# Kernel optimization log

Hardware: AMD Instinct MI355X
Metric: run time of the kernel (lower is better)

## Reference

```python
import jax, jax.numpy as jnp
import numpy as np

BETA = 0.95
THRESH = 1.0
T = 25
MAXD = 11      # dilated_kernel_size: 250//25=10 -> bumped to odd 11
LP = 10        # left_pad = 250//25
B = 1024
SIGINIT = 5.0  # max_delay // 2, SIG is frozen at this value


@jax.custom_vjp
def atan_spike(u):
    # heaviside forward, atan surrogate gradient (snntorch surrogate.atan, alpha=2)
    return (u > 0).astype(u.dtype)

def _atan_fwd(u):
    return atan_spike(u), u

def _atan_bwd(u, g):
    return (g / (1.0 + (jnp.pi * u) ** 2),)

atan_spike.defvjp(_atan_fwd, _atan_bwd)


def dcls_kernel(W, P, SIG):
    # DCLS 'gauss': gaussian-interpolated dense kernel.
    # W: (O, I, kc), P/SIG: (1, O, I, kc) -> dense kernel (O, I, MAXD)
    idx = jnp.arange(MAXD, dtype=W.dtype)
    Pc = P[0] + MAXD // 2                      # center positions in dense kernel
    S = jnp.abs(SIG[0]) + 0.27                 # sigma floor (DCLS epsilon)
    X = jnp.exp(-0.5 * ((idx[:, None, None, None] - Pc) / S) ** 2)  # (K,O,I,kc)
    X = X / (X.sum(axis=0, keepdims=True) + 1e-7)
    return jnp.einsum('oic,joic->oij', W, X)


def dcls_conv(x, W, P, SIG, b):
    # x: (B, C_in, L) -> (B, C_out, L - MAXD + 1), VALID conv like padding=0
    k = dcls_kernel(W, P, SIG)
    y = jax.lax.conv_general_dilated(x, k, (1,), 'VALID',
                                     dimension_numbers=('NCH', 'OIH', 'NCH'))
    return y + b[None, :, None]


def batchnorm(x, gamma, beta, mean, var, eps=1e-5):
    # eval-mode BatchNorm1d over (B, C, L)
    inv = gamma / jnp.sqrt(var + eps)
    return (x - mean[None, :, None]) * inv[None, :, None] + beta[None, :, None]


def lif_scan(x):
    # snntorch Leaky, reset_mechanism='subtract'; x: (B, C, T) input currents
    xT = jnp.moveaxis(x, 2, 0)  # (T, B, C)

    def step(mem, xt):
        reset = jax.lax.stop_gradient(atan_spike(mem - THRESH))  # detached reset
        mem = BETA * mem + xt - reset * THRESH
        spk = atan_spike(mem - THRESH)
        return mem, (spk, mem)

    _, (spk, mem) = jax.lax.scan(step, jnp.zeros_like(xT[0]), xT)
    return spk, mem  # each (T, B, C)


def pad_left(x):
    return jnp.pad(x, ((0, 0), (0, 0), (LP, 0)))


def setup_inputs() -> dict:
    key = jax.random.key(0)
    ks = jax.random.split(key, 16)

    def w_init(k, o, i):
        return jax.random.normal(k, (o, i, 1), jnp.float32) / np.sqrt(i)

    inp = {
        'data': jax.random.normal(ks[0], (B, T, 140), jnp.float32),
        'W1': w_init(ks[1], 256, 140),
        'b1': jax.random.normal(ks[2], (256,), jnp.float32) * 0.01,
        'P1': jax.random.uniform(ks[3], (1, 256, 140, 1), jnp.float32, -SIGINIT, SIGINIT),
        'SIG1': jnp.full((1, 256, 140, 1), SIGINIT, jnp.float32),
        'bn1_gamma': jax.random.uniform(ks[4], (256,), jnp.float32, 0.5, 1.5),
        'bn1_beta': jax.random.normal(ks[5], (256,), jnp.float32) * 0.1,
        'bn1_mean': jax.random.normal(ks[6], (256,), jnp.float32) * 0.1,
        'bn1_var': jax.random.uniform(ks[7], (256,), jnp.float32, 0.5, 1.5),
        'W2': w_init(ks[8], 256, 256),
        'b2': jax.random.normal(ks[9], (256,), jnp.float32) * 0.01,
        'P2': jax.random.uniform(ks[10], (1, 256, 256, 1), jnp.float32, -SIGINIT, SIGINIT),
        'SIG2': jnp.full((1, 256, 256, 1), SIGINIT, jnp.float32),
        'bn2_gamma': jax.random.uniform(ks[11], (256,), jnp.float32, 0.5, 1.5),
        'bn2_beta': jax.random.normal(ks[12], (256,), jnp.float32) * 0.1,
        'bn2_mean': jax.random.normal(ks[13], (256,), jnp.float32) * 0.1,
        'bn2_var': jax.random.uniform(ks[14], (256,), jnp.float32, 0.5, 1.5),
        'W3': w_init(ks[15], 20, 256),
        'b3': jnp.zeros((20,), jnp.float32),
        'P3': jax.random.uniform(jax.random.fold_in(key, 99), (1, 20, 256, 1), jnp.float32, -SIGINIT, SIGINIT),
        'SIG3': jnp.full((1, 20, 256, 1), SIGINIT, jnp.float32),
    }
    return inp


def reference(data, W1, b1, P1, SIG1, bn1_gamma, bn1_beta, bn1_mean, bn1_var,
              W2, b2, P2, SIG2, bn2_gamma, bn2_beta, bn2_mean, bn2_var,
              W3, b3, P3, SIG3):
    # data: (B, T, 140); pad time dim on the left, then to (B, C, L)
    x = jnp.moveaxis(jnp.pad(data, ((0, 0), (LP, 0), (0, 0))), 1, 2)  # (B,140,T+LP)
    x = batchnorm(dcls_conv(x, W1, P1, SIG1, b1), bn1_gamma, bn1_beta, bn1_mean, bn1_var)
    spk1, _ = lif_scan(x)                  # (T, B, 256)
    in1 = jnp.moveaxis(spk1, 0, 2)         # (B, 256, T)  (dropout eval = identity)

    x = batchnorm(dcls_conv(pad_left(in1), W2, P2, SIG2, b2),
                  bn2_gamma, bn2_beta, bn2_mean, bn2_var)
    spk2, _ = lif_scan(x)
    in2 = jnp.moveaxis(spk2, 0, 2)         # (B, 256, T)

    x = dcls_conv(pad_left(in2), W3, P3, SIG3, b3)  # (B, 20, T)
    spk3, mem3 = lif_scan(x)               # (T, B, 20) each
    return spk3, mem3
```

## Files before the change

kernel.cpp:

```cpp
#include <hip/hip_runtime.h>
#include <math.h>

#define BB 1024
#define TT 25
#define LP 10
#define MAXD 11

#define XR2 26
#define XC 264
#define XSZ2 (XR2 * XC)

#define IC1 140
#define ICP1 160
#define XC1 168
#define XSZ1 (XR2 * XC1)
#define SS1 (2 * XSZ1)

typedef __bf16 bf16x8 __attribute__((ext_vector_type(8)));
typedef float  f32x4  __attribute__((ext_vector_type(4)));

#define MFMA16(A, B, C) __builtin_amdgcn_mfma_f32_16x16x32_bf16((A), (B), (C), 0, 0, 0)

__global__ void gen_trip(const float* __restrict__ W,
                         const float* __restrict__ P,
                         const float* __restrict__ SIG,
                         __bf16* __restrict__ Khi, __bf16* __restrict__ Kmid,
                         __bf16* __restrict__ Klo,
                         int O, int Opad, int I, int Ipad) {
    int idx = blockIdx.x * blockDim.x + threadIdx.x;
    if (idx >= Opad * Ipad) return;
    int i = idx % Ipad;
    int o = idx / Ipad;
    if (o >= O || i >= I) {
#pragma unroll
        for (int j = 0; j < MAXD; ++j) {
            size_t ofs = ((size_t)(j * Opad + o)) * Ipad + i;
            Khi[ofs] = (__bf16)0.0f;
            Kmid[ofs] = (__bf16)0.0f;
            Klo[ofs] = (__bf16)0.0f;
        }
        return;
    }
    int widx = o * I + i;
    float w  = W[widx];
    float pc = P[widx] + (float)(MAXD / 2);
    float s  = fabsf(SIG[widx]) + 0.27f;
    float x[MAXD];
    float sum = 0.f;
#pragma unroll
    for (int j = 0; j < MAXD; ++j) {
        float d = ((float)j - pc) / s;
        x[j] = expf(-0.5f * d * d);
        sum += x[j];
    }
    float denom = sum + 1e-7f;
#pragma unroll
    for (int j = 0; j < MAXD; ++j) {
        float kv = w * (x[j] / denom);
        __bf16 h = (__bf16)kv;
        float  r1 = kv - (float)h;
        __bf16 m = (__bf16)r1;
        float  r2 = r1 - (float)m;
        __bf16 l = (__bf16)r2;
        size_t ofs = ((size_t)(j * Opad + o)) * Ipad + i;
        Khi[ofs] = h;
        Kmid[ofs] = m;
        Klo[ofs] = l;
    }
}

__global__ __launch_bounds__(512, 2)
void conv1_mfma(const float* __restrict__ xin,
                const __bf16* __restrict__ Khi,
                const __bf16* __restrict__ Kmid,
                const __bf16* __restrict__ Klo,
                const float* __restrict__ bias,
                const float* __restrict__ gamma,
                const float* __restrict__ beta,
                const float* __restrict__ mean,
                const float* __restrict__ var,
                __bf16* __restrict__ spk1) {
    __shared__ __align__(16) char smem[3 * SS1 * 2];
    __bf16* xs = (__bf16*)smem;
    float*  ys = (float*)smem;

    const int rr = blockIdx.x & 7;
    const int gg = blockIdx.x >> 3;
    const int pp = 2 * (rr + 8 * (gg >> 1)) + (gg & 1);
    const int b0 = pp * 2;

    const int tid  = threadIdx.x;
    const int w    = tid >> 6;
    const int lane = tid & 63;
    const int lm   = lane & 15;
    const int quad = lane >> 4;

    {
        uint32_t* xz = (uint32_t*)smem;
        for (int k = tid; k < 3 * SS1 / 2; k += 512) xz[k] = 0u;
    }
    __syncthreads();
#pragma unroll
    for (int bl = 0; bl < 2; ++bl) {
        const float* src = xin + (size_t)(b0 + bl) * (TT * IC1);
        for (int k = tid; k < TT * IC1; k += 512) {
            int t = k / IC1;
            int i = k - t * IC1;
            float x  = src[k];
            __bf16 h = (__bf16)x;
            float r1 = x - (float)h;
            __bf16 m = (__bf16)r1;
            float r2 = r1 - (float)m;
            __bf16 l = (__bf16)r2;
            int ofs = bl * XSZ1 + t * XC1 + i;
            xs[0 * SS1 + ofs] = h;
            xs[1 * SS1 + ofs] = m;
            xs[2 * SS1 + ofs] = l;
        }
    }
    __syncthreads();

    f32x4 acc[2][4];
#pragma unroll
    for (int p = 0; p < 2; ++p)
#pragma unroll
        for (int nt = 0; nt < 4; ++nt) acc[p][nt] = (f32x4){0.f, 0.f, 0.f, 0.f};

    auto loadA = [&](int n, bf16x8* Ah, bf16x8* Am, bf16x8* Al) {
        n = (n > 54) ? 54 : n;
        const int j = n / 5;
        const int ic = n - 5 * j;
        const size_t base =
            (size_t)(j * 256 + w * 32 + lm) * ICP1 + ic * 32 + quad * 8;
#pragma unroll
        for (int p = 0; p < 2; ++p) {
            Ah[p] = *(const bf16x8*)(Khi  + base + p * 16 * ICP1);
            Am[p] = *(const bf16x8*)(Kmid + base + p * 16 * ICP1);
            Al[p] = *(const bf16x8*)(Klo  + base + p * 16 * ICP1);
        }
    };

    auto step = [&](int n, bf16x8* Ah, bf16x8* Am, bf16x8* Al) {
        const int j = n / 5;
        const int ic = n - 5 * j;
        int r0 = lm + j - 10;          r0 = ((unsigned)r0 < 25u) ? r0 : 25;
        int r1 = 16 + lm + j - 10;     r1 = ((unsigned)r1 < 25u) ? r1 : 25;
        const int col = ic * 32 + quad * 8;
#pragma unroll
        for (int bl = 0; bl < 2; ++bl) {
            bf16x8 Bh[2], Bm[2], Bl[2];
#pragma unroll
            for (int th = 0; th < 2; ++th) {
                const int row = th ? r1 : r0;
                const int ofs = bl * XSZ1 + row * XC1 + col;
                Bh[th] = *(const bf16x8*)&xs[0 * SS1 + ofs];
                Bm[th] = *(const bf16x8*)&xs[1 * SS1 + ofs];
                Bl[th] = *(const bf16x8*)&xs[2 * SS1 + ofs];
            }
#pragma unroll
            for (int p = 0; p < 2; ++p)
#pragma unroll
                for (int th = 0; th < 2; ++th)
                    acc[p][bl * 2 + th] = MFMA16(Ah[p], Bh[th], acc[p][bl * 2 + th]);
#pragma unroll
            for (int p = 0; p < 2; ++p)
#pragma unroll
                for (int th = 0; th < 2; ++th)
                    acc[p][bl * 2 + th] = MFMA16(Ah[p], Bm[th], acc[p][bl * 2 + th]);
#pragma unroll
            for (int p = 0; p < 2; ++p)
#pragma unroll
                for (int th = 0; th < 2; ++th)
                    acc[p][bl * 2 + th] = MFMA16(Am[p], Bh[th], acc[p][bl * 2 + th]);
#pragma unroll
            for (int p = 0; p < 2; ++p)
#pragma unroll
                for (int th = 0; th < 2; ++th)
                    acc[p][bl * 2 + th] = MFMA16(Ah[p], Bl[th], acc[p][bl * 2 + th]);
#pragma unroll
            for (int p = 0; p < 2; ++p)
#pragma unroll
                for (int th = 0; th < 2; ++th)
                    acc[p][bl * 2 + th] = MFMA16(Am[p], Bm[th], acc[p][bl * 2 + th]);
#pragma unroll
            for (int p = 0; p < 2; ++p)
#pragma unroll
                for (int th = 0; th < 2; ++th)
                    acc[p][bl * 2 + th] = MFMA16(Al[p], Bh[th], acc[p][bl * 2 + th]);
        }
    };

    bf16x8 A0h[2], A0m[2], A0l[2], A1h[2], A1m[2], A1l[2];
    loadA(0, A0h, A0m, A0l);
    for (int n = 0; n < 54; n += 2) {
        loadA(n + 1, A1h, A1m, A1l);
        step(n, A0h, A0m, A0l);
        loadA(n + 2, A0h, A0m, A0l);
        step(n + 1, A1h, A1m, A1l);
    }
    step(54, A0h, A0m, A0l);

#pragma unroll
    for (int bl = 0; bl < 2; ++bl) {
        __syncthreads();
#pragma unroll
        for (int p = 0; p < 2; ++p)
#pragma unroll
            for (int th = 0; th < 2; ++th) {
                int t = th * 16 + lm;
                if (t < TT) {
                    int ob = w * 32 + p * 16 + quad * 4;
#pragma unroll
                    for (int v = 0; v < 4; ++v)
                        ys[(ob + v) * 27 + t] = acc[p][bl * 2 + th][v];
                }
            }
        __syncthreads();
        if (tid < 256) {
            const int o = tid;
            float scale = gamma[o] / sqrtf(var[o] + 1e-5f);
            float ofs   = (bias[o] - mean[o]) * scale + beta[o];
            unsigned short* dst =
                (unsigned short*)spk1 + (size_t)(b0 + bl) * (TT * 256) + o;
            const float* yrow = &ys[o * 27];
            float memv = 0.f;
#pragma unroll
            for (int t = 0; t < TT; ++t) {
                float a     = yrow[t] * scale + ofs;
                float reset = (memv > 1.0f) ? 1.0f : 0.f;
                memv        = 0.95f * memv + a - reset;
                dst[t * 256] = (memv > 1.0f) ? 0x3F80 : 0;
            }
        }
    }
}

__global__ __launch_bounds__(512, 2)
void conv2_mfma(const __bf16* __restrict__ spk1,
                const __bf16* __restrict__ Khi,
                const __bf16* __restrict__ Kmid,
                const __bf16* __restrict__ Klo,
                const float* __restrict__ bias,
                const float* __restrict__ gamma,
                const float* __restrict__ beta,
                const float* __restrict__ mean,
                const float* __restrict__ var,
                __bf16* __restrict__ spk2) {
    __shared__ __align__(16) char smem[116480];
    __bf16* xs  = (__bf16*)smem;
    float*  ysq = (float*)(smem + 109824);

    const int h    = blockIdx.x & 1;
    const int bg   = blockIdx.x >> 1;
    const int b0   = bg * 8;
    const int oc0  = h * 128;

    const int tid  = threadIdx.x;
    const int w    = tid >> 6;
    const int wc   = w & 3;
    const int wb   = w >> 2;
    const int lane = tid & 63;
    const int lm   = lane & 15;
    const int quad = lane >> 4;

    for (int k = tid; k < 8 * (XC / 2); k += 512) {
        int bl = k / (XC / 2);
        int c  = k % (XC / 2);
        ((uint32_t*)xs)[(bl * XSZ2 + 25 * XC) / 2 + c] = 0u;
    }
    for (int k = tid; k < 8 * 800; k += 512) {
        int bl = k / 800;
        int v  = k % 800;
        int t  = v >> 5;
        int iv = v & 31;
        uint4 d = ((const uint4*)(spk1 + (size_t)(b0 + bl) * (TT * 256)))[v];
        *(uint4*)&xs[bl * XSZ2 + t * XC + iv * 8] = d;
    }
    __syncthreads();

    f32x4 acc[2][8];
#pragma unroll
    for (int pi = 0; pi < 2; ++pi)
#pragma unroll
        for (int nt = 0; nt < 8; ++nt) acc[pi][nt] = (f32x4){0.f, 0.f, 0.f, 0.f};

    {
        auto loadA = [&](int n, bf16x8* Ah, bf16x8* Am, bf16x8* Al) {
            n = (n > 87) ? 87 : n;
            const int j = n >> 3, ic = n & 7;
#pragma unroll
            for (int pi = 0; pi < 2; ++pi) {
                const size_t base =
                    (size_t)(j * 256 + oc0 + wc * 32 + pi * 16 + lm) * 256 +
                    ic * 32 + quad * 8;
                Ah[pi] = *(const bf16x8*)(Khi  + base);
                Am[pi] = *(const bf16x8*)(Kmid + base);
                Al[pi] = *(const bf16x8*)(Klo  + base);
            }
        };
        auto step = [&](int n, bf16x8* Ah, bf16x8* Am, bf16x8* Al) {
            const int j = n >> 3, ic = n & 7;
            int r0 = lm + j - 10;          r0 = ((unsigned)r0 < 25u) ? r0 : 25;
            int r1 = 16 + lm + j - 10;     r1 = ((unsigned)r1 < 25u) ? r1 : 25;
            const int col = ic * 32 + quad * 8;
            bf16x8 Bf[8];
#pragma unroll
            for (int bl = 0; bl < 4; ++bl) {
                const int xb = wb * 4 + bl;
                Bf[bl * 2 + 0] = *(const bf16x8*)&xs[xb * XSZ2 + r0 * XC + col];
                Bf[bl * 2 + 1] = *(const bf16x8*)&xs[xb * XSZ2 + r1 * XC + col];
            }
#pragma unroll
            for (int pi = 0; pi < 2; ++pi)
#pragma unroll
                for (int nt = 0; nt < 8; ++nt)
                    acc[pi][nt] = MFMA16(Ah[pi], Bf[nt], acc[pi][nt]);
#pragma unroll
            for (int pi = 0; pi < 2; ++pi)
#pragma unroll
                for (int nt = 0; nt < 8; ++nt)
                    acc[pi][nt] = MFMA16(Am[pi], Bf[nt], acc[pi][nt]);
#pragma unroll
            for (int pi = 0; pi < 2; ++pi)
#pragma unroll
                for (int nt = 0; nt < 8; ++nt)
                    acc[pi][nt] = MFMA16(Al[pi], Bf[nt], acc[pi][nt]);
        };

        bf16x8 A0h[2], A0m[2], A0l[2], A1h[2], A1m[2], A1l[2];
        loadA(0, A0h, A0m, A0l);
        for (int n = 0; n < 86; n += 2) {
            loadA(n + 1, A1h, A1m, A1l);
            step(n, A0h, A0m, A0l);
            loadA(n + 2, A0h, A0m, A0l);
            step(n + 1, A1h, A1m, A1l);
        }
        loadA(87, A1h, A1m, A1l);
        step(86, A0h, A0m, A0l);
        step(87, A1h, A1m, A1l);
    }

#pragma unroll
    for (int blg = 0; blg < 8; ++blg) {
#pragma unroll
        for (int q = 0; q < 2; ++q) {
            __syncthreads();
            if (wb == (blg >> 2) && (wc >> 1) == q) {
#pragma unroll
                for (int pi = 0; pi < 2; ++pi)
#pragma unroll
                    for (int th = 0; th < 2; ++th) {
                        int t = th * 16 + lm;
                        if (t < TT) {
                            int ol = (wc & 1) * 32 + pi * 16 + quad * 4;
#pragma unroll
                            for (int v = 0; v < 4; ++v)
                                ysq[(ol + v) * 26 + t] =
                                    acc[pi][(blg & 3) * 2 + th][v];
                        }
                    }
            }
            __syncthreads();
            if (tid < 64) {
                const int o = oc0 + q * 64 + tid;
                float scale = gamma[o] / sqrtf(var[o] + 1e-5f);
                float ofs   = (bias[o] - mean[o]) * scale + beta[o];
                const float* yrow = &ysq[tid * 26];
                unsigned short* dst =
                    (unsigned short*)spk2 + (size_t)(b0 + blg) * (TT * 256) + o;
                float memv = 0.f;
#pragma unroll
                for (int t = 0; t < TT; ++t) {
                    float a     = yrow[t] * scale + ofs;
                    float reset = (memv > 1.0f) ? 1.0f : 0.f;
                    memv        = 0.95f * memv + a - reset;
                    dst[t * 256] = (memv > 1.0f) ? 0x3F80 : 0;
                }
            }
        }
    }
}

__global__ __launch_bounds__(512, 2)
void conv3_mfma(const __bf16* __restrict__ spk2,
                const __bf16* __restrict__ K3hi,
                const __bf16* __restrict__ K3mid,
                const __bf16* __restrict__ K3lo,
                const float* __restrict__ b3,
                float* __restrict__ out) {
    __shared__ __align__(16) char smem[54912];
    __bf16* xs  = (__bf16*)smem;
    float*  ys3 = (float*)smem;

    const int b0   = blockIdx.x * 4;
    const int tid  = threadIdx.x;
    const int w    = tid >> 6;
    const int lane = tid & 63;
    const int lm   = lane & 15;
    const int quad = lane >> 4;

    for (int k = tid; k < 4 * (XC / 2); k += 512) {
        int bl = k / (XC / 2);
        int c  = k % (XC / 2);
        ((uint32_t*)xs)[(bl * XSZ2 + 25 * XC) / 2 + c] = 0u;
    }
    for (int k = tid; k < 4 * 800; k += 512) {
        int bl = k / 800;
        int v  = k % 800;
        int t  = v >> 5;
        int iv = v & 31;
        uint4 d = ((const uint4*)(spk2 + (size_t)(b0 + bl) * (TT * 256)))[v];
        *(uint4*)&xs[bl * XSZ2 + t * XC + iv * 8] = d;
    }
    __syncthreads();

    {
        const int p3  = w >> 2;
        const int bl3 = w & 3;
        f32x4 accH[2], accM[2], accL[2];
#pragma unroll
        for (int th = 0; th < 2; ++th) {
            accH[th] = (f32x4){0.f, 0.f, 0.f, 0.f};
            accM[th] = (f32x4){0.f, 0.f, 0.f, 0.f};
            accL[th] = (f32x4){0.f, 0.f, 0.f, 0.f};
        }

        auto loadA3 = [&](int n, bf16x8* Ah, bf16x8* Am, bf16x8* Al) {
            n = (n > 87) ? 87 : n;
            const int j = n >> 3, ic = n & 7;
            const size_t kofs =
                ((size_t)(j * 32 + p3 * 16 + lm)) * 256 + ic * 32 + quad * 8;
            *Ah = *(const bf16x8*)(K3hi  + kofs);
            *Am = *(const bf16x8*)(K3mid + kofs);
            *Al = *(const bf16x8*)(K3lo  + kofs);
        };
        auto step3 = [&](int n, bf16x8 Ah, bf16x8 Am, bf16x8 Al) {
            const int j = n >> 3, ic = n & 7;
#pragma unroll
            for (int th = 0; th < 2; ++th) {
                int r = th * 16 + lm + j - 10;
                r = ((unsigned)r < 25u) ? r : 25;
                bf16x8 Bf =
                    *(const bf16x8*)&xs[bl3 * XSZ2 + r * XC + ic * 32 + quad * 8];
                accH[th] = MFMA16(Ah, Bf, accH[th]);
                accM[th] = MFMA16(Am, Bf, accM[th]);
                accL[th] = MFMA16(Al, Bf, accL[th]);
            }
        };

        bf16x8 A0h, A0m, A0l, A1h, A1m, A1l;
        loadA3(0, &A0h, &A0m, &A0l);
        for (int n = 0; n < 86; n += 2) {
            loadA3(n + 1, &A1h, &A1m, &A1l);
            step3(n, A0h, A0m, A0l);
            loadA3(n + 2, &A0h, &A0m, &A0l);
            step3(n + 1, A1h, A1m, A1l);
        }
        loadA3(87, &A1h, &A1m, &A1l);
        step3(86, A0h, A0m, A0l);
        step3(87, A1h, A1m, A1l);

        __syncthreads();
#pragma unroll
        for (int th = 0; th < 2; ++th) {
            int t = th * 16 + lm;
            if (t < TT) {
#pragma unroll
                for (int v = 0; v < 4; ++v)
                    ys3[(bl3 * 32 + p3 * 16 + quad * 4 + v) * 26 + t] =
                        accH[th][v] + accM[th][v] + accL[th][v];
            }
        }
        __syncthreads();

        if (tid < 80) {
            const int bl2 = tid / 20;
            const int o   = tid % 20;
            float memv = 0.f;
            float bo   = b3[o];
            const float* yrow = &ys3[(bl2 * 32 + o) * 26];
#pragma unroll
            for (int t = 0; t < TT; ++t) {
                float a     = yrow[t] + bo;
                float reset = (memv > 1.0f) ? 1.0f : 0.f;
                memv        = 0.95f * memv + a - reset;
                float spk   = (memv > 1.0f) ? 1.0f : 0.f;
                out[(t * BB + (b0 + bl2)) * 20 + o]               = spk;
                out[TT * BB * 20 + (t * BB + (b0 + bl2)) * 20 + o] = memv;
            }
        }
    }
}

extern "C" void kernel_launch(void* const* d_in, const int* in_sizes, int n_in,
                              void* d_out, int out_size, void* d_ws, size_t ws_size,
                              hipStream_t stream) {
    const float* data = (const float*)d_in[0];
    const float* W1   = (const float*)d_in[1];
    const float* b1   = (const float*)d_in[2];
    const float* P1   = (const float*)d_in[3];
    const float* SIG1 = (const float*)d_in[4];
    const float* g1   = (const float*)d_in[5];
    const float* be1  = (const float*)d_in[6];
    const float* m1   = (const float*)d_in[7];
    const float* v1   = (const float*)d_in[8];
    const float* W2   = (const float*)d_in[9];
    const float* b2   = (const float*)d_in[10];
    const float* P2   = (const float*)d_in[11];
    const float* SIG2 = (const float*)d_in[12];
    const float* g2   = (const float*)d_in[13];
    const float* be2  = (const float*)d_in[14];
    const float* m2   = (const float*)d_in[15];
    const float* v2   = (const float*)d_in[16];
    const float* W3   = (const float*)d_in[17];
    const float* b3   = (const float*)d_in[18];
    const float* P3   = (const float*)d_in[19];
    const float* SIG3 = (const float*)d_in[20];
    float* out = (float*)d_out;

    char* p = (char*)d_ws;
    __bf16* K1hi  = (__bf16*)p;  p += 901120;
    __bf16* K1mid = (__bf16*)p;  p += 901120;
    __bf16* K1lo  = (__bf16*)p;  p += 901120;
    __bf16* spk1  = (__bf16*)p;  p += 13107200;
    __bf16* K2hi  = (__bf16*)p;  p += 1441792;
    __bf16* K2mid = (__bf16*)p;  p += 1441792;
    __bf16* K2lo  = (__bf16*)p;  p += 1441792;
    __bf16* K3hi  = (__bf16*)p;  p += 180224;
    __bf16* K3mid = (__bf16*)p;  p += 180224;
    __bf16* K3lo  = (__bf16*)p;  p += 180224;
    __bf16* spk2  = (__bf16*)p;

    gen_trip<<<(256 * 160 + 255) / 256, 256, 0, stream>>>(
        W1, P1, SIG1, K1hi, K1mid, K1lo, 256, 256, 140, 160);
    gen_trip<<<(256 * 256 + 255) / 256, 256, 0, stream>>>(
        W2, P2, SIG2, K2hi, K2mid, K2lo, 256, 256, 256, 256);
    gen_trip<<<(32 * 256 + 255) / 256, 256, 0, stream>>>(
        W3, P3, SIG3, K3hi, K3mid, K3lo, 20, 32, 256, 256);

    conv1_mfma<<<BB / 2, 512, 0, stream>>>(data, K1hi, K1mid, K1lo,
                                           b1, g1, be1, m1, v1, spk1);
    conv2_mfma<<<BB / 4, 512, 0, stream>>>(spk1, K2hi, K2mid, K2lo,
                                           b2, g2, be2, m2, v2, spk2);
    conv3_mfma<<<BB / 4, 512, 0, stream>>>(spk2, K3hi, K3mid, K3lo, b3, out);
}
```

Measured before the change: 432.1 us.

## Split conv2 reduction across wave groups with 4-batch blocks and more occupancy

conv2 now handles 4 batch rows per block instead of 8, launches twice as many blocks, and splits the 88-step K reduction between two wave groups. Their partial sums are added in shared memory before the LIF scan. Shared memory drops from about 116KB to 68KB and launch bounds rise to 4 blocks per CU, aiming for more concurrent waves and better latency hiding. The explicit double-buffered A-fragment prefetch is removed in favour of loads interleaved between MFMA groups. Each weight fragment is now reused across fewer batches, so more global weight traffic is needed per unit of work.

Measured after the change: 465.5 us. 1.08x slower.

```diff
diff --git a/kernel.cpp b/kernel.cpp
--- a/kernel.cpp
+++ b/kernel.cpp
@@ -235,7 +235,7 @@
     }
 }
 
-__global__ __launch_bounds__(512, 2)
+__global__ __launch_bounds__(512, 4)
 void conv2_mfma(const __bf16* __restrict__ spk1,
                 const __bf16* __restrict__ Khi,
                 const __bf16* __restrict__ Kmid,
@@ -246,29 +246,29 @@
                 const float* __restrict__ mean,
                 const float* __restrict__ var,
                 __bf16* __restrict__ spk2) {
-    __shared__ __align__(16) char smem[116480];
+    __shared__ __align__(16) char smem[68224];
     __bf16* xs  = (__bf16*)smem;
-    float*  ysq = (float*)(smem + 109824);
+    float*  ysq = (float*)(smem + 54912);
 
     const int h    = blockIdx.x & 1;
     const int bg   = blockIdx.x >> 1;
-    const int b0   = bg * 8;
+    const int b0   = bg * 4;
     const int oc0  = h * 128;
 
     const int tid  = threadIdx.x;
     const int w    = tid >> 6;
     const int wc   = w & 3;
-    const int wb   = w >> 2;
+    const int kg   = w >> 2;
     const int lane = tid & 63;
     const int lm   = lane & 15;
     const int quad = lane >> 4;
 
-    for (int k = tid; k < 8 * (XC / 2); k += 512) {
+    for (int k = tid; k < 4 * (XC / 2); k += 512) {
         int bl = k / (XC / 2);
         int c  = k % (XC / 2);
         ((uint32_t*)xs)[(bl * XSZ2 + 25 * XC) / 2 + c] = 0u;
     }
-    for (int k = tid; k < 8 * 800; k += 512) {
+    for (int k = tid; k < 4 * 800; k += 512) {
         int bl = k / 800;
         int v  = k % 800;
         int t  = v >> 5;
@@ -285,20 +285,9 @@
         for (int nt = 0; nt < 8; ++nt) acc[pi][nt] = (f32x4){0.f, 0.f, 0.f, 0.f};
 
     {
-        auto loadA = [&](int n, bf16x8* Ah, bf16x8* Am, bf16x8* Al) {
-            n = (n > 87) ? 87 : n;
-            const int j = n >> 3, ic = n & 7;
-#pragma unroll
-            for (int pi = 0; pi < 2; ++pi) {
-                const size_t base =
-                    (size_t)(j * 256 + oc0 + wc * 32 + pi * 16 + lm) * 256 +
-                    ic * 32 + quad * 8;
-                Ah[pi] = *(const bf16x8*)(Khi  + base);
-                Am[pi] = *(const bf16x8*)(Kmid + base);
-                Al[pi] = *(const bf16x8*)(Klo  + base);
-            }
-        };
-        auto step = [&](int n, bf16x8* Ah, bf16x8* Am, bf16x8* Al) {
+        const int n0 = kg * 44;
+#pragma unroll 2
+        for (int n = n0; n < n0 + 44; ++n) {
             const int j = n >> 3, ic = n & 7;
             int r0 = lm + j - 10;          r0 = ((unsigned)r0 < 25u) ? r0 : 25;
             int r1 = 16 + lm + j - 10;     r1 = ((unsigned)r1 < 25u) ? r1 : 25;
@@ -306,10 +295,15 @@
             bf16x8 Bf[8];
 #pragma unroll
             for (int bl = 0; bl < 4; ++bl) {
-                const int xb = wb * 4 + bl;
-                Bf[bl * 2 + 0] = *(const bf16x8*)&xs[xb * XSZ2 + r0 * XC + col];
-                Bf[bl * 2 + 1] = *(const bf16x8*)&xs[xb * XSZ2 + r1 * XC + col];
-            }
+                Bf[bl * 2 + 0] = *(const bf16x8*)&xs[bl * XSZ2 + r0 * XC + col];
+                Bf[bl * 2 + 1] = *(const bf16x8*)&xs[bl * XSZ2 + r1 * XC + col];
+            }
+            const size_t base =
+                (size_t)(j * 256 + oc0 + wc * 32 + lm) * 256 + ic * 32 + quad * 8;
+            bf16x8 Ah[2], Am[2], Al[2];
+#pragma unroll
+            for (int pi = 0; pi < 2; ++pi)
+                Ah[pi] = *(const bf16x8*)(Khi + base + pi * 16 * 256);
 #pragma unroll
             for (int pi = 0; pi < 2; ++pi)
 #pragma unroll
@@ -317,35 +311,29 @@
                     acc[pi][nt] = MFMA16(Ah[pi], Bf[nt], acc[pi][nt]);
 #pragma unroll
             for (int pi = 0; pi < 2; ++pi)
+                Am[pi] = *(const bf16x8*)(Kmid + base + pi * 16 * 256);
+#pragma unroll
+            for (int pi = 0; pi < 2; ++pi)
 #pragma unroll
                 for (int nt = 0; nt < 8; ++nt)
                     acc[pi][nt] = MFMA16(Am[pi], Bf[nt], acc[pi][nt]);
 #pragma unroll
             for (int pi = 0; pi < 2; ++pi)
+                Al[pi] = *(const bf16x8*)(Klo + base + pi * 16 * 256);
+#pragma unroll
+            for (int pi = 0; pi < 2; ++pi)
 #pragma unroll
                 for (int nt = 0; nt < 8; ++nt)
                     acc[pi][nt] = MFMA16(Al[pi], Bf[nt], acc[pi][nt]);
-        };
-
-        bf16x8 A0h[2], A0m[2], A0l[2], A1h[2], A1m[2], A1l[2];
-        loadA(0, A0h, A0m, A0l);
-        for (int n = 0; n < 86; n += 2) {
-            loadA(n + 1, A1h, A1m, A1l);
-            step(n, A0h, A0m, A0l);
-            loadA(n + 2, A0h, A0m, A0l);
-            step(n + 1, A1h, A1m, A1l);
-        }
-        loadA(87, A1h, A1m, A1l);
-        step(86, A0h, A0m, A0l);
-        step(87, A1h, A1m, A1l);
-    }
-
-#pragma unroll
-    for (int blg = 0; blg < 8; ++blg) {
+        }
+    }
+
+#pragma unroll
+    for (int bl = 0; bl < 4; ++bl) {
 #pragma unroll
         for (int q = 0; q < 2; ++q) {
             __syncthreads();
-            if (wb == (blg >> 2) && (wc >> 1) == q) {
+            if ((wc >> 1) == q) {
 #pragma unroll
                 for (int pi = 0; pi < 2; ++pi)
 #pragma unroll
@@ -355,8 +343,8 @@
                             int ol = (wc & 1) * 32 + pi * 16 + quad * 4;
 #pragma unroll
                             for (int v = 0; v < 4; ++v)
-                                ysq[(ol + v) * 26 + t] =
-                                    acc[pi][(blg & 3) * 2 + th][v];
+                                ysq[(kg * 64 + ol + v) * 26 + t] =
+                                    acc[pi][bl * 2 + th][v];
                         }
                     }
             }
@@ -365,13 +353,14 @@
                 const int o = oc0 + q * 64 + tid;
                 float scale = gamma[o] / sqrtf(var[o] + 1e-5f);
                 float ofs   = (bias[o] - mean[o]) * scale + beta[o];
-                const float* yrow = &ysq[tid * 26];
+                const float* yr0 = &ysq[tid * 26];
+                const float* yr1 = &ysq[(64 + tid) * 26];
                 unsigned short* dst =
-                    (unsigned short*)spk2 + (size_t)(b0 + blg) * (TT * 256) + o;
+                    (unsigned short*)spk2 + (size_t)(b0 + bl) * (TT * 256) + o;
                 float memv = 0.f;
 #pragma unroll
                 for (int t = 0; t < TT; ++t) {
-                    float a     = yrow[t] * scale + ofs;
+                    float a     = (yr0[t] + yr1[t]) * scale + ofs;
                     float reset = (memv > 1.0f) ? 1.0f : 0.f;
                     memv        = 0.95f * memv + a - reset;
                     dst[t * 256] = (memv > 1.0f) ? 0x3F80 : 0;
@@ -540,7 +529,7 @@
 
     conv1_mfma<<<BB / 2, 512, 0, stream>>>(data, K1hi, K1mid, K1lo,
                                            b1, g1, be1, m1, v1, spk1);
-    conv2_mfma<<<BB / 4, 512, 0, stream>>>(spk1, K2hi, K2mid, K2lo,
+    conv2_mfma<<<BB / 2, 512, 0, stream>>>(spk1, K2hi, K2mid, K2lo,
                                            b2, g2, be2, m2, v2, spk2);
     conv3_mfma<<<BB / 4, 512, 0, stream>>>(spk2, K3hi, K3mid, K3lo, b3, out);
 }
```
